# Kernel optimization log

Measured on AMD Instinct MI355X. Metric: run time of the kernel, lower is better.

Reference implementation:

```python
import jax, jax.numpy as jnp
import numpy as np

# Module hyperparameters (from __init__ defaults / init_kwargs)
A_PLUS = 0.005
A_MINUS = 0.00525
TAU_PLUS = 20.0
TAU_MINUS = 20.0
DT = 1.0

B, T, N_PRE, N_POST = 512, 100, 256, 256
SPIKE_RATE = 0.1


def setup_inputs() -> dict:
    key = jax.random.key(0)
    k1, k2, k3 = jax.random.split(key, 3)
    pre_spikes = (jax.random.uniform(k1, (B, T, N_PRE)) < SPIKE_RATE).astype(jnp.float32)
    post_spikes = (jax.random.uniform(k2, (B, T, N_POST)) < SPIKE_RATE).astype(jnp.float32)
    weights = jax.random.uniform(k3, (N_PRE, N_POST), dtype=jnp.float32)
    return {"pre_spikes": pre_spikes, "post_spikes": post_spikes, "weights": weights}


def _pre_trace(pre_tbn, decay):
    """trace[t] = sum_{tau=1..t} decay^tau * pre[t-tau]  (exact recurrence).

    pre_tbn: [T, B, N]. Returns [T, B, N] with trace[0] = 0.
    """
    def step(carry, x_t):
        # emit trace[t] = carry, then carry' = decay * (carry + pre[t])
        return decay * (carry + x_t), carry
    _, trace = jax.lax.scan(step, jnp.zeros_like(pre_tbn[0]), pre_tbn)
    return trace


def reference(pre_spikes, post_spikes, weights):
    """Classical STDP weight update.

    With T <= int(tau_plus*5) the original nested t/tau loops equal:
      dW[p,q] = (1/(B*T)) * sum_{t,b} (A+ * trace+[t,b,p] - A- * trace-[t,b,p]) * post[b,t,q]
    where trace+/- are exponential pre-synaptic eligibility traces.
    """
    batch, time_steps, _ = pre_spikes.shape
    pre_t = jnp.transpose(pre_spikes, (1, 0, 2))    # [T, B, n_pre]
    post_t = jnp.transpose(post_spikes, (1, 0, 2))  # [T, B, n_post]

    decay_plus = jnp.exp(jnp.float32(-DT / TAU_PLUS))
    decay_minus = jnp.exp(jnp.float32(-DT / TAU_MINUS))

    trace_plus = _pre_trace(pre_t, decay_plus)    # LTP: pre fires before post
    trace_minus = _pre_trace(pre_t, decay_minus)  # LTD: pre fires before post (depression of reversed pairing)

    eff = A_PLUS * trace_plus - A_MINUS * trace_minus  # [T, B, n_pre]
    weight_update = jnp.einsum('tbp,tbq->pq', eff, post_t) / (batch * time_steps)
    # original initializes update as zeros_like(weights); output shape matches weights
    return weight_update + jnp.zeros_like(weights)
```

## Files before the change

kernel.cpp:

```cpp
#include <hip/hip_runtime.h>
#include <stdint.h>

#define B_SZ   512
#define T_SZ   100
#define NPRE   256
#define NPOST  256
#define KTOT   (B_SZ * T_SZ)

typedef __bf16 bf16x8 __attribute__((ext_vector_type(8)));
typedef float  floatx4 __attribute__((ext_vector_type(4)));

__device__ __forceinline__ uint32_t bf16_rne(float v) {
    uint32_t bits = __float_as_uint(v);
    return (bits + 0x7FFFu + ((bits >> 16) & 1u)) >> 16;
}
__device__ __forceinline__ uint32_t pack_trunc2(float a, float b) {
    return (__float_as_uint(a) >> 16) | (__float_as_uint(b) & 0xFFFF0000u);
}

__global__ __launch_bounds__(512, 4) void stdp_fused_gemm(
    const float* __restrict__ pre, const float* __restrict__ post,
    float* __restrict__ partial)
{
    __shared__ __align__(16) unsigned short A_lds[32][512];
    __shared__ __align__(16) unsigned short B_lds[32][512];

    const int bx   = blockIdx.x;
    const int s    = bx & 127;
    const int tile = bx >> 7;
    const int pt   = tile & 1;
    const int qt   = tile >> 1;
    const int tid  = threadIdx.x;
    const int lane = tid & 63, wave = tid >> 6;
    const int l15 = lane & 15, l4 = lane >> 4;

    const int grp   = tid >> 7;
    const int p_loc = tid & 127;
    const int qloc  = tid & 127;
    const int qg = qloc >> 4, q15 = qloc & 15;
    const int pg = p_loc >> 4, lp = p_loc & 15;

    const float decay = 0.95122942450071400910f;

    uint32_t pk[50];
    {
        const int b = s * 4 + grp;
        const float* src = pre + (size_t)b * (T_SZ * NPRE) + pt * 128 + p_loc;
        float carry = 0.0f;
#pragma unroll
        for (int kc = 0; kc < 3; ++kc) {
            float x[32];
#pragma unroll
            for (int j = 0; j < 32; ++j)
                x[j] = src[(size_t)(kc * 32 + j) * NPRE];
#pragma unroll
            for (int j = 0; j < 16; ++j) {
                uint32_t lo = bf16_rne(carry);
                carry = decay * (carry + x[2 * j]);
                uint32_t hi = bf16_rne(carry);
                carry = decay * (carry + x[2 * j + 1]);
                pk[kc * 16 + j] = lo | (hi << 16);
            }
        }
        float x[4];
#pragma unroll
        for (int j = 0; j < 4; ++j)
            x[j] = src[(size_t)(96 + j) * NPRE];
#pragma unroll
        for (int j = 0; j < 2; ++j) {
            uint32_t lo = bf16_rne(carry);
            carry = decay * (carry + x[2 * j]);
            uint32_t hi = bf16_rne(carry);
            carry = decay * (carry + x[2 * j + 1]);
            pk[48 + j] = lo | (hi << 16);
        }
    }

    floatx4 acc[8] = {};

#pragma unroll
    for (int g = 0; g < 4; ++g) {
        const int b = s * 4 + g;
        if (g) __syncthreads();

        if (grp == g) {
#pragma unroll
            for (int kc = 0; kc < 3; ++kc)
#pragma unroll
                for (int w = 0; w < 4; ++w)
                    *(uint4*)&A_lds[kc * 8 + pg][(w * 16 + lp) * 8] =
                        make_uint4(pk[kc * 16 + w * 4],     pk[kc * 16 + w * 4 + 1],
                                   pk[kc * 16 + w * 4 + 2], pk[kc * 16 + w * 4 + 3]);
            *(uint4*)&A_lds[24 + pg][lp * 8] = make_uint4(pk[48], pk[49], 0u, 0u);
#pragma unroll
            for (int w = 1; w < 4; ++w)
                *(uint4*)&A_lds[24 + pg][(w * 16 + lp) * 8] =
                    make_uint4(0u, 0u, 0u, 0u);
        }

        const float* pb = post + (size_t)b * (T_SZ * NPOST) + qt * 128 + qloc;
        if (grp < 3) {
#pragma unroll
            for (int h = 0; h < 2; ++h) {
                float x[16];
#pragma unroll
                for (int j = 0; j < 16; ++j)
                    x[j] = pb[(size_t)(grp * 32 + h * 16 + j) * NPOST];
#pragma unroll
                for (int w2 = 0; w2 < 2; ++w2) {
                    const int w = h * 2 + w2;
                    *(uint4*)&B_lds[grp * 8 + qg][(w * 16 + q15) * 8] =
                        make_uint4(pack_trunc2(x[w2 * 8 + 0], x[w2 * 8 + 1]),
                                   pack_trunc2(x[w2 * 8 + 2], x[w2 * 8 + 3]),
                                   pack_trunc2(x[w2 * 8 + 4], x[w2 * 8 + 5]),
                                   pack_trunc2(x[w2 * 8 + 6], x[w2 * 8 + 7]));
                }
            }
        } else {
            float x[4];
#pragma unroll
            for (int j = 0; j < 4; ++j)
                x[j] = pb[(size_t)(96 + j) * NPOST];
            *(uint4*)&B_lds[24 + qg][q15 * 8] =
                make_uint4(pack_trunc2(x[0], x[1]), pack_trunc2(x[2], x[3]), 0u, 0u);
#pragma unroll
            for (int w = 1; w < 4; ++w)
                *(uint4*)&B_lds[24 + qg][(w * 16 + q15) * 8] =
                    make_uint4(0u, 0u, 0u, 0u);
        }
        __syncthreads();

#pragma unroll
        for (int kc = 0; kc < 4; ++kc) {
            bf16x8 a = *(const bf16x8*)&A_lds[kc * 8 + wave][lane * 8];
            bf16x8 bb[8];
#pragma unroll
            for (int gg = 0; gg < 8; ++gg)
                bb[gg] = *(const bf16x8*)&B_lds[kc * 8 + gg][lane * 8];
#pragma unroll
            for (int gg = 0; gg < 8; ++gg)
                acc[gg] = __builtin_amdgcn_mfma_f32_16x16x32_bf16(
                    a, bb[gg], acc[gg], 0, 0, 0);
        }
    }

    float* pout = partial + (size_t)bx * (128 * 128);
    const int r0 = wave * 16 + l4 * 4;
#pragma unroll
    for (int gg = 0; gg < 8; ++gg) {
        const int c = gg * 16 + l15;
#pragma unroll
        for (int v = 0; v < 4; ++v)
            pout[(size_t)(r0 + v) * 128 + c] = acc[gg][v];
    }
}

__global__ __launch_bounds__(256) void stdp_reduce1(
    const float* __restrict__ partial, float* __restrict__ tmp)
{
    const int t = blockIdx.x * 256 + threadIdx.x;
    const int g = t >> 16;
    const int e = t & 65535;
    const int tile = e >> 14;
    const float* src = partial + ((size_t)(tile * 128 + g * 16) << 14) + (e & 16383);
    float a4[4] = {};
#pragma unroll
    for (int i = 0; i < 4; ++i)
#pragma unroll
        for (int u = 0; u < 4; ++u)
            a4[u] += src[(size_t)(u * 4 + i) << 14];
    tmp[t] = (a4[0] + a4[1]) + (a4[2] + a4[3]);
}

__global__ __launch_bounds__(256) void stdp_reduce2(
    const float* __restrict__ tmp, float* __restrict__ out)
{
    const int idx = blockIdx.x * 256 + threadIdx.x;
    const int P = idx >> 8, Q = idx & 255;
    const int tile = (Q >> 7) * 2 + (P >> 7);
    const int e = (tile << 14) | ((P & 127) << 7) | (Q & 127);
    float a[4];
#pragma unroll
    for (int u = 0; u < 4; ++u)
        a[u] = tmp[(size_t)(2 * u) * 65536 + e] +
               tmp[(size_t)(2 * u + 1) * 65536 + e];
    const float scale = (0.005f - 0.00525f) * (1.0f / (float)KTOT);
    out[idx] = ((a[0] + a[1]) + (a[2] + a[3])) * scale;
}

extern "C" void kernel_launch(void* const* d_in, const int* in_sizes, int n_in,
                              void* d_out, int out_size, void* d_ws, size_t ws_size,
                              hipStream_t stream)
{
    const float* pre  = (const float*)d_in[0];
    const float* post = (const float*)d_in[1];
    float* out = (float*)d_out;

    float* partial = (float*)d_ws;
    float* tmp     = (float*)((char*)d_ws + (size_t)33554432);

    stdp_fused_gemm<<<512, 512, 0, stream>>>(pre, post, partial);
    stdp_reduce1<<<2048, 256, 0, stream>>>(partial, tmp);
    stdp_reduce2<<<256, 256, 0, stream>>>(tmp, out);
}
```

Measured before the change: 145.8 us.

## Double-buffer LDS tiles and use 1024-thread blocks covering eight batches each

The GEMM kernel now launches 256 blocks of 1024 threads. Each block handles eight batch items instead of four, and each wave computes a 16x64 output slice instead of 16x128. LDS tiles are double-buffered, so the next batch's post-spike loads are issued before the current MFMA work, which removes one barrier per step. With half as many blocks, the partial-sum buffer is halved and the first reduction reads fewer slices. The risks are lower occupancy from 1024-thread blocks and twice the LDS per block.

```diff
diff --git a/kernel.cpp b/kernel.cpp
--- a/kernel.cpp
+++ b/kernel.cpp
@@ -18,16 +18,69 @@
     return (__float_as_uint(a) >> 16) | (__float_as_uint(b) & 0xFFFF0000u);
 }
 
-__global__ __launch_bounds__(512, 4) void stdp_fused_gemm(
+__device__ __forceinline__ void deposit_A(unsigned short (*A)[512],
+                                          const uint32_t* pk, int pg, int lp)
+{
+#pragma unroll
+    for (int kc = 0; kc < 3; ++kc)
+#pragma unroll
+        for (int w = 0; w < 4; ++w)
+            *(uint4*)&A[kc * 8 + pg][(w * 16 + lp) * 8] =
+                make_uint4(pk[kc * 16 + w * 4],     pk[kc * 16 + w * 4 + 1],
+                           pk[kc * 16 + w * 4 + 2], pk[kc * 16 + w * 4 + 3]);
+    *(uint4*)&A[24 + pg][lp * 8] = make_uint4(pk[48], pk[49], 0u, 0u);
+#pragma unroll
+    for (int w = 1; w < 4; ++w)
+        *(uint4*)&A[24 + pg][(w * 16 + lp) * 8] = make_uint4(0u, 0u, 0u, 0u);
+}
+
+__device__ __forceinline__ void load_B(const float* pb, int grp, float* x)
+{
+    if (grp < 6) {
+#pragma unroll
+        for (int j = 0; j < 16; ++j)
+            x[j] = pb[(size_t)(16 * grp + j) * NPOST];
+    } else if (grp == 6) {
+#pragma unroll
+        for (int j = 0; j < 4; ++j)
+            x[j] = pb[(size_t)(96 + j) * NPOST];
+    }
+}
+__device__ __forceinline__ void store_B(unsigned short (*Bl)[512], int grp,
+                                        int qg, int q15, const float* x)
+{
+    if (grp < 6) {
+#pragma unroll
+        for (int h = 0; h < 2; ++h) {
+            const int o = 2 * grp + h;
+            *(uint4*)&Bl[(o >> 2) * 8 + qg][((o & 3) * 16 + q15) * 8] =
+                make_uint4(pack_trunc2(x[8 * h + 0], x[8 * h + 1]),
+                           pack_trunc2(x[8 * h + 2], x[8 * h + 3]),
+                           pack_trunc2(x[8 * h + 4], x[8 * h + 5]),
+                           pack_trunc2(x[8 * h + 6], x[8 * h + 7]));
+        }
+    } else if (grp == 6) {
+        *(uint4*)&Bl[24 + qg][q15 * 8] =
+            make_uint4(pack_trunc2(x[0], x[1]), pack_trunc2(x[2], x[3]), 0u, 0u);
+    } else {
+#pragma unroll
+        for (int o = 13; o < 16; ++o)
+            *(uint4*)&Bl[24 + qg][((o & 3) * 16 + q15) * 8] =
+                make_uint4(0u, 0u, 0u, 0u);
+    }
+}
+
+__global__ __launch_bounds__(1024) __attribute__((amdgpu_waves_per_eu(4, 4)))
+void stdp_fused_gemm(
     const float* __restrict__ pre, const float* __restrict__ post,
     float* __restrict__ partial)
 {
-    __shared__ __align__(16) unsigned short A_lds[32][512];
-    __shared__ __align__(16) unsigned short B_lds[32][512];
+    __shared__ __align__(16) unsigned short A_lds[2][32][512];
+    __shared__ __align__(16) unsigned short B_lds[2][32][512];
 
     const int bx   = blockIdx.x;
-    const int s    = bx & 127;
-    const int tile = bx >> 7;
+    const int s    = bx & 63;
+    const int tile = bx >> 6;
     const int pt   = tile & 1;
     const int qt   = tile >> 1;
     const int tid  = threadIdx.x;
@@ -39,12 +92,15 @@
     const int qloc  = tid & 127;
     const int qg = qloc >> 4, q15 = qloc & 15;
     const int pg = p_loc >> 4, lp = p_loc & 15;
+    const int wpg = wave >> 1;
+    const int wqh = wave & 1;
 
     const float decay = 0.95122942450071400910f;
+    const int b0 = s * 8;
 
     uint32_t pk[50];
     {
-        const int b = s * 4 + grp;
+        const int b = b0 + grp;
         const float* src = pre + (size_t)b * (T_SZ * NPRE) + pt * 128 + p_loc;
         float carry = 0.0f;
 #pragma unroll
@@ -76,79 +132,51 @@
         }
     }
 
-    floatx4 acc[8] = {};
-
-#pragma unroll
-    for (int g = 0; g < 4; ++g) {
-        const int b = s * 4 + g;
-        if (g) __syncthreads();
-
-        if (grp == g) {
-#pragma unroll
-            for (int kc = 0; kc < 3; ++kc)
-#pragma unroll
-                for (int w = 0; w < 4; ++w)
-                    *(uint4*)&A_lds[kc * 8 + pg][(w * 16 + lp) * 8] =
-                        make_uint4(pk[kc * 16 + w * 4],     pk[kc * 16 + w * 4 + 1],
-                                   pk[kc * 16 + w * 4 + 2], pk[kc * 16 + w * 4 + 3]);
-            *(uint4*)&A_lds[24 + pg][lp * 8] = make_uint4(pk[48], pk[49], 0u, 0u);
-#pragma unroll
-            for (int w = 1; w < 4; ++w)
-                *(uint4*)&A_lds[24 + pg][(w * 16 + lp) * 8] =
-                    make_uint4(0u, 0u, 0u, 0u);
-        }
-
-        const float* pb = post + (size_t)b * (T_SZ * NPOST) + qt * 128 + qloc;
-        if (grp < 3) {
-#pragma unroll
-            for (int h = 0; h < 2; ++h) {
-                float x[16];
-#pragma unroll
-                for (int j = 0; j < 16; ++j)
-                    x[j] = pb[(size_t)(grp * 32 + h * 16 + j) * NPOST];
-#pragma unroll
-                for (int w2 = 0; w2 < 2; ++w2) {
-                    const int w = h * 2 + w2;
-                    *(uint4*)&B_lds[grp * 8 + qg][(w * 16 + q15) * 8] =
-                        make_uint4(pack_trunc2(x[w2 * 8 + 0], x[w2 * 8 + 1]),
-                                   pack_trunc2(x[w2 * 8 + 2], x[w2 * 8 + 3]),
-                                   pack_trunc2(x[w2 * 8 + 4], x[w2 * 8 + 5]),
-                                   pack_trunc2(x[w2 * 8 + 6], x[w2 * 8 + 7]));
-                }
-            }
-        } else {
-            float x[4];
-#pragma unroll
-            for (int j = 0; j < 4; ++j)
-                x[j] = pb[(size_t)(96 + j) * NPOST];
-            *(uint4*)&B_lds[24 + qg][q15 * 8] =
-                make_uint4(pack_trunc2(x[0], x[1]), pack_trunc2(x[2], x[3]), 0u, 0u);
-#pragma unroll
-            for (int w = 1; w < 4; ++w)
-                *(uint4*)&B_lds[24 + qg][(w * 16 + q15) * 8] =
-                    make_uint4(0u, 0u, 0u, 0u);
-        }
-        __syncthreads();
+    floatx4 acc[4] = {};
+
+    if (grp == 0) deposit_A(A_lds[0], pk, pg, lp);
+    {
+        float xb[16];
+        load_B(post + (size_t)b0 * (T_SZ * NPOST) + qt * 128 + qloc, grp, xb);
+        store_B(B_lds[0], grp, qg, q15, xb);
+    }
+    __syncthreads();
+
+#pragma unroll
+    for (int g = 0; g < 8; ++g) {
+        const int nb = g + 1;
+        const int cb = g & 1;
+
+        float xn[16];
+        if (nb < 8)
+            load_B(post + (size_t)(b0 + nb) * (T_SZ * NPOST) + qt * 128 + qloc,
+                   grp, xn);
 
 #pragma unroll
         for (int kc = 0; kc < 4; ++kc) {
-            bf16x8 a = *(const bf16x8*)&A_lds[kc * 8 + wave][lane * 8];
-            bf16x8 bb[8];
-#pragma unroll
-            for (int gg = 0; gg < 8; ++gg)
-                bb[gg] = *(const bf16x8*)&B_lds[kc * 8 + gg][lane * 8];
-#pragma unroll
-            for (int gg = 0; gg < 8; ++gg)
+            bf16x8 a = *(const bf16x8*)&A_lds[cb][kc * 8 + wpg][lane * 8];
+            bf16x8 bb[4];
+#pragma unroll
+            for (int gg = 0; gg < 4; ++gg)
+                bb[gg] = *(const bf16x8*)&B_lds[cb][kc * 8 + wqh * 4 + gg][lane * 8];
+#pragma unroll
+            for (int gg = 0; gg < 4; ++gg)
                 acc[gg] = __builtin_amdgcn_mfma_f32_16x16x32_bf16(
                     a, bb[gg], acc[gg], 0, 0, 0);
         }
+
+        if (nb < 8) {
+            if (grp == nb) deposit_A(A_lds[nb & 1], pk, pg, lp);
+            store_B(B_lds[nb & 1], grp, qg, q15, xn);
+            __syncthreads();
+        }
     }
 
     float* pout = partial + (size_t)bx * (128 * 128);
-    const int r0 = wave * 16 + l4 * 4;
-#pragma unroll
-    for (int gg = 0; gg < 8; ++gg) {
-        const int c = gg * 16 + l15;
+    const int r0 = wpg * 16 + l4 * 4;
+#pragma unroll
+    for (int gg = 0; gg < 4; ++gg) {
+        const int c = (wqh * 4 + gg) * 16 + l15;
 #pragma unroll
         for (int v = 0; v < 4; ++v)
             pout[(size_t)(r0 + v) * 128 + c] = acc[gg][v];
@@ -162,13 +190,13 @@
     const int g = t >> 16;
     const int e = t & 65535;
     const int tile = e >> 14;
-    const float* src = partial + ((size_t)(tile * 128 + g * 16) << 14) + (e & 16383);
+    const float* src = partial + ((size_t)(tile * 64 + g * 8) << 14) + (e & 16383);
     float a4[4] = {};
 #pragma unroll
-    for (int i = 0; i < 4; ++i)
+    for (int i = 0; i < 2; ++i)
 #pragma unroll
         for (int u = 0; u < 4; ++u)
-            a4[u] += src[(size_t)(u * 4 + i) << 14];
+            a4[u] += src[(size_t)(u * 2 + i) << 14];
     tmp[t] = (a4[0] + a4[1]) + (a4[2] + a4[3]);
 }
 
@@ -197,9 +225,9 @@
     float* out = (float*)d_out;
 
     float* partial = (float*)d_ws;
-    float* tmp     = (float*)((char*)d_ws + (size_t)33554432);
-
-    stdp_fused_gemm<<<512, 512, 0, stream>>>(pre, post, partial);
+    float* tmp     = (float*)((char*)d_ws + (size_t)16777216);
+
+    stdp_fused_gemm<<<256, 1024, 0, stream>>>(pre, post, partial);
     stdp_reduce1<<<2048, 256, 0, stream>>>(partial, tmp);
     stdp_reduce2<<<256, 256, 0, stream>>>(tmp, out);
 }
```

Result: no change. 144.2 us (-1.1%).

## Compute full 256x256 tile per block with double-buffered LDS staging

Applied to the files above, without the earlier changes.

The GEMM kernel now uses 1024-thread blocks. Each block covers the full 256x256 output for two batches instead of one 128x128 quadrant for four batches. Each input row is therefore read and trace-processed once rather than twice, using float2/float4 vectorized loads. A two-buffer LDS pipeline overlaps staging of the next 32-step chunk with the MFMA work on the current one. The cost is a per-block partial output twice as large, which doubles the traffic of the reduction kernels. Only 6 of the 16 waves do the serial trace and conversion staging, which could leave the pipeline latency-bound.

```diff
diff --git a/kernel.cpp b/kernel.cpp
--- a/kernel.cpp
+++ b/kernel.cpp
@@ -18,141 +18,144 @@
     return (__float_as_uint(a) >> 16) | (__float_as_uint(b) & 0xFFFF0000u);
 }
 
-__global__ __launch_bounds__(512, 4) void stdp_fused_gemm(
+__global__ __launch_bounds__(1024, 4) void stdp_fused_gemm(
     const float* __restrict__ pre, const float* __restrict__ post,
     float* __restrict__ partial)
 {
-    __shared__ __align__(16) unsigned short A_lds[32][512];
-    __shared__ __align__(16) unsigned short B_lds[32][512];
+    __shared__ __align__(16) unsigned short A_lds[2][16][512];
+    __shared__ __align__(16) unsigned short B_lds[2][16][512];
 
     const int bx   = blockIdx.x;
-    const int s    = bx & 127;
-    const int tile = bx >> 7;
-    const int pt   = tile & 1;
-    const int qt   = tile >> 1;
     const int tid  = threadIdx.x;
     const int lane = tid & 63, wave = tid >> 6;
     const int l15 = lane & 15, l4 = lane >> 4;
 
-    const int grp   = tid >> 7;
-    const int p_loc = tid & 127;
-    const int qloc  = tid & 127;
-    const int qg = qloc >> 4, q15 = qloc & 15;
-    const int pg = p_loc >> 4, lp = p_loc & 15;
-
     const float decay = 0.95122942450071400910f;
-
-    uint32_t pk[50];
-    {
-        const int b = s * 4 + grp;
-        const float* src = pre + (size_t)b * (T_SZ * NPRE) + pt * 128 + p_loc;
-        float carry = 0.0f;
-#pragma unroll
-        for (int kc = 0; kc < 3; ++kc) {
-            float x[32];
-#pragma unroll
-            for (int j = 0; j < 32; ++j)
-                x[j] = src[(size_t)(kc * 32 + j) * NPRE];
-#pragma unroll
-            for (int j = 0; j < 16; ++j) {
-                uint32_t lo = bf16_rne(carry);
-                carry = decay * (carry + x[2 * j]);
-                uint32_t hi = bf16_rne(carry);
-                carry = decay * (carry + x[2 * j + 1]);
-                pk[kc * 16 + j] = lo | (hi << 16);
-            }
+    const int b0 = 2 * bx;
+
+    float c0 = 0.0f, c1 = 0.0f;
+
+    const int p0  = (wave & 1) * 128 + 2 * lane;
+    const int apg = p0 >> 4, ap15 = p0 & 15;
+    const int bg  = wave - 2;
+    const int qg  = lane >> 2, q15 = (4 * lane) & 15;
+
+    floatx4 acc[4][4] = {};
+
+#define STAGE_A(BUF, BT, CK)                                                   \
+    {                                                                          \
+        const int b_ = b0 + (BT);                                              \
+        if ((CK) == 0) { c0 = 0.0f; c1 = 0.0f; }                               \
+        const float* rb_ = pre + (size_t)b_ * (T_SZ * NPRE) +                  \
+                           (wave & 1) * 128 + 2 * lane;                        \
+        _Pragma("unroll")                                                      \
+        for (int og_ = 0; og_ < 4; ++og_) {                                    \
+            float xx_[16];                                                     \
+            _Pragma("unroll")                                                  \
+            for (int j_ = 0; j_ < 8; ++j_) {                                   \
+                const int t_ = (CK) * 32 + og_ * 8 + j_;                       \
+                if (t_ < T_SZ) {                                               \
+                    float2 v_ = *(const float2*)(rb_ + (size_t)t_ * NPRE);     \
+                    xx_[2 * j_] = v_.x; xx_[2 * j_ + 1] = v_.y;                \
+                } else { xx_[2 * j_] = 0.0f; xx_[2 * j_ + 1] = 0.0f; }         \
+            }                                                                  \
+            uint32_t u0_[4], u1_[4];                                           \
+            _Pragma("unroll")                                                  \
+            for (int m_ = 0; m_ < 4; ++m_) {                                   \
+                uint32_t lo0_ = bf16_rne(c0);                                  \
+                c0 = decay * (c0 + xx_[4 * m_ + 0]);                           \
+                uint32_t lo1_ = bf16_rne(c1);                                  \
+                c1 = decay * (c1 + xx_[4 * m_ + 1]);                           \
+                uint32_t hi0_ = bf16_rne(c0);                                  \
+                c0 = decay * (c0 + xx_[4 * m_ + 2]);                           \
+                uint32_t hi1_ = bf16_rne(c1);                                  \
+                c1 = decay * (c1 + xx_[4 * m_ + 3]);                           \
+                u0_[m_] = lo0_ | (hi0_ << 16);                                 \
+                u1_[m_] = lo1_ | (hi1_ << 16);                                 \
+            }                                                                  \
+            *(uint4*)&A_lds[BUF][apg][(og_ * 16 + ap15) * 8] =                 \
+                make_uint4(u0_[0], u0_[1], u0_[2], u0_[3]);                    \
+            *(uint4*)&A_lds[BUF][apg][(og_ * 16 + ap15 + 1) * 8] =             \
+                make_uint4(u1_[0], u1_[1], u1_[2], u1_[3]);                    \
+        }                                                                      \
+    }
+
+#define STAGE_B(BUF, BT, CK)                                                   \
+    {                                                                          \
+        const int b_ = b0 + (BT);                                              \
+        const float* rb_ = post + (size_t)b_ * (T_SZ * NPOST) + 4 * lane;      \
+        float xx_[8][4];                                                       \
+        _Pragma("unroll")                                                      \
+        for (int j_ = 0; j_ < 8; ++j_) {                                       \
+            const int t_ = (CK) * 32 + bg * 8 + j_;                            \
+            if (t_ < T_SZ) {                                                   \
+                float4 v_ = *(const float4*)(rb_ + (size_t)t_ * NPOST);        \
+                xx_[j_][0] = v_.x; xx_[j_][1] = v_.y;                          \
+                xx_[j_][2] = v_.z; xx_[j_][3] = v_.w;                          \
+            } else {                                                           \
+                xx_[j_][0] = 0.0f; xx_[j_][1] = 0.0f;                          \
+                xx_[j_][2] = 0.0f; xx_[j_][3] = 0.0f;                          \
+            }                                                                  \
+        }                                                                      \
+        _Pragma("unroll")                                                      \
+        for (int c_ = 0; c_ < 4; ++c_) {                                       \
+            uint32_t u_[4];                                                    \
+            _Pragma("unroll")                                                  \
+            for (int m_ = 0; m_ < 4; ++m_)                                     \
+                u_[m_] = pack_trunc2(xx_[2 * m_][c_], xx_[2 * m_ + 1][c_]);    \
+            *(uint4*)&B_lds[BUF][qg][(bg * 16 + q15 + c_) * 8] =               \
+                make_uint4(u_[0], u_[1], u_[2], u_[3]);                        \
+        }                                                                      \
+    }
+
+#define MFMA_STEP(BUF)                                                         \
+    {                                                                          \
+        bf16x8 af_[4], bf_[4];                                                 \
+        _Pragma("unroll")                                                      \
+        for (int f_ = 0; f_ < 4; ++f_) {                                       \
+            af_[f_] = *(const bf16x8*)&A_lds[BUF][(wave >> 2) * 4 + f_]        \
+                                           [lane * 8];                         \
+            bf_[f_] = *(const bf16x8*)&B_lds[BUF][(wave & 3) * 4 + f_]         \
+                                           [lane * 8];                         \
+        }                                                                      \
+        _Pragma("unroll")                                                      \
+        for (int fa_ = 0; fa_ < 4; ++fa_)                                      \
+            _Pragma("unroll")                                                  \
+            for (int fb_ = 0; fb_ < 4; ++fb_)                                  \
+                acc[fa_][fb_] = __builtin_amdgcn_mfma_f32_16x16x32_bf16(       \
+                    af_[fa_], bf_[fb_], acc[fa_][fb_], 0, 0, 0);               \
+    }
+
+    if (wave < 2)      STAGE_A(0, 0, 0)
+    else if (wave < 6) STAGE_B(0, 0, 0)
+    __syncthreads();
+
+#pragma unroll
+    for (int k = 0; k < 8; ++k) {
+        const int cur = k & 1, nxt = cur ^ 1;
+        if (k < 7) {
+            if (wave < 2)      STAGE_A(nxt, (k + 1) >> 2, (k + 1) & 3)
+            else if (wave < 6) STAGE_B(nxt, (k + 1) >> 2, (k + 1) & 3)
         }
-        float x[4];
-#pragma unroll
-        for (int j = 0; j < 4; ++j)
-            x[j] = src[(size_t)(96 + j) * NPRE];
-#pragma unroll
-        for (int j = 0; j < 2; ++j) {
-            uint32_t lo = bf16_rne(carry);
-            carry = decay * (carry + x[2 * j]);
-            uint32_t hi = bf16_rne(carry);
-            carry = decay * (carry + x[2 * j + 1]);
-            pk[48 + j] = lo | (hi << 16);
+        MFMA_STEP(cur)
+        __syncthreads();
+    }
+
+    float* pout = partial + (size_t)bx * (256 * 256);
+#pragma unroll
+    for (int fa = 0; fa < 4; ++fa) {
+        const int r0 = (wave >> 2) * 64 + fa * 16 + l4 * 4;
+#pragma unroll
+        for (int fb = 0; fb < 4; ++fb) {
+            const int c = (wave & 3) * 64 + fb * 16 + l15;
+#pragma unroll
+            for (int v = 0; v < 4; ++v)
+                pout[(size_t)(r0 + v) * 256 + c] = acc[fa][fb][v];
         }
     }
-
-    floatx4 acc[8] = {};
-
-#pragma unroll
-    for (int g = 0; g < 4; ++g) {
-        const int b = s * 4 + g;
-        if (g) __syncthreads();
-
-        if (grp == g) {
-#pragma unroll
-            for (int kc = 0; kc < 3; ++kc)
-#pragma unroll
-                for (int w = 0; w < 4; ++w)
-                    *(uint4*)&A_lds[kc * 8 + pg][(w * 16 + lp) * 8] =
-                        make_uint4(pk[kc * 16 + w * 4],     pk[kc * 16 + w * 4 + 1],
-                                   pk[kc * 16 + w * 4 + 2], pk[kc * 16 + w * 4 + 3]);
-            *(uint4*)&A_lds[24 + pg][lp * 8] = make_uint4(pk[48], pk[49], 0u, 0u);
-#pragma unroll
-            for (int w = 1; w < 4; ++w)
-                *(uint4*)&A_lds[24 + pg][(w * 16 + lp) * 8] =
-                    make_uint4(0u, 0u, 0u, 0u);
-        }
-
-        const float* pb = post + (size_t)b * (T_SZ * NPOST) + qt * 128 + qloc;
-        if (grp < 3) {
-#pragma unroll
-            for (int h = 0; h < 2; ++h) {
-                float x[16];
-#pragma unroll
-                for (int j = 0; j < 16; ++j)
-                    x[j] = pb[(size_t)(grp * 32 + h * 16 + j) * NPOST];
-#pragma unroll
-                for (int w2 = 0; w2 < 2; ++w2) {
-                    const int w = h * 2 + w2;
-                    *(uint4*)&B_lds[grp * 8 + qg][(w * 16 + q15) * 8] =
-                        make_uint4(pack_trunc2(x[w2 * 8 + 0], x[w2 * 8 + 1]),
-                                   pack_trunc2(x[w2 * 8 + 2], x[w2 * 8 + 3]),
-                                   pack_trunc2(x[w2 * 8 + 4], x[w2 * 8 + 5]),
-                                   pack_trunc2(x[w2 * 8 + 6], x[w2 * 8 + 7]));
-                }
-            }
-        } else {
-            float x[4];
-#pragma unroll
-            for (int j = 0; j < 4; ++j)
-                x[j] = pb[(size_t)(96 + j) * NPOST];
-            *(uint4*)&B_lds[24 + qg][q15 * 8] =
-                make_uint4(pack_trunc2(x[0], x[1]), pack_trunc2(x[2], x[3]), 0u, 0u);
-#pragma unroll
-            for (int w = 1; w < 4; ++w)
-                *(uint4*)&B_lds[24 + qg][(w * 16 + q15) * 8] =
-                    make_uint4(0u, 0u, 0u, 0u);
-        }
-        __syncthreads();
-
-#pragma unroll
-        for (int kc = 0; kc < 4; ++kc) {
-            bf16x8 a = *(const bf16x8*)&A_lds[kc * 8 + wave][lane * 8];
-            bf16x8 bb[8];
-#pragma unroll
-            for (int gg = 0; gg < 8; ++gg)
-                bb[gg] = *(const bf16x8*)&B_lds[kc * 8 + gg][lane * 8];
-#pragma unroll
-            for (int gg = 0; gg < 8; ++gg)
-                acc[gg] = __builtin_amdgcn_mfma_f32_16x16x32_bf16(
-                    a, bb[gg], acc[gg], 0, 0, 0);
-        }
-    }
-
-    float* pout = partial + (size_t)bx * (128 * 128);
-    const int r0 = wave * 16 + l4 * 4;
-#pragma unroll
-    for (int gg = 0; gg < 8; ++gg) {
-        const int c = gg * 16 + l15;
-#pragma unroll
-        for (int v = 0; v < 4; ++v)
-            pout[(size_t)(r0 + v) * 128 + c] = acc[gg][v];
-    }
+#undef STAGE_A
+#undef STAGE_B
+#undef MFMA_STEP
 }
 
 __global__ __launch_bounds__(256) void stdp_reduce1(
@@ -161,14 +164,13 @@
     const int t = blockIdx.x * 256 + threadIdx.x;
     const int g = t >> 16;
     const int e = t & 65535;
-    const int tile = e >> 14;
-    const float* src = partial + ((size_t)(tile * 128 + g * 16) << 14) + (e & 16383);
+    const float* src = partial + ((size_t)g * 32) * 65536 + e;
     float a4[4] = {};
 #pragma unroll
-    for (int i = 0; i < 4; ++i)
+    for (int i = 0; i < 8; ++i)
 #pragma unroll
         for (int u = 0; u < 4; ++u)
-            a4[u] += src[(size_t)(u * 4 + i) << 14];
+            a4[u] += src[(size_t)(i * 4 + u) * 65536];
     tmp[t] = (a4[0] + a4[1]) + (a4[2] + a4[3]);
 }
 
@@ -176,14 +178,11 @@
     const float* __restrict__ tmp, float* __restrict__ out)
 {
     const int idx = blockIdx.x * 256 + threadIdx.x;
-    const int P = idx >> 8, Q = idx & 255;
-    const int tile = (Q >> 7) * 2 + (P >> 7);
-    const int e = (tile << 14) | ((P & 127) << 7) | (Q & 127);
     float a[4];
 #pragma unroll
     for (int u = 0; u < 4; ++u)
-        a[u] = tmp[(size_t)(2 * u) * 65536 + e] +
-               tmp[(size_t)(2 * u + 1) * 65536 + e];
+        a[u] = tmp[(size_t)(2 * u) * 65536 + idx] +
+               tmp[(size_t)(2 * u + 1) * 65536 + idx];
     const float scale = (0.005f - 0.00525f) * (1.0f / (float)KTOT);
     out[idx] = ((a[0] + a[1]) + (a[2] + a[3])) * scale;
 }
@@ -197,9 +196,9 @@
     float* out = (float*)d_out;
 
     float* partial = (float*)d_ws;
-    float* tmp     = (float*)((char*)d_ws + (size_t)33554432);
-
-    stdp_fused_gemm<<<512, 512, 0, stream>>>(pre, post, partial);
+    float* tmp     = (float*)((char*)d_ws + (size_t)67108864);
+
+    stdp_fused_gemm<<<256, 1024, 0, stream>>>(pre, post, partial);
     stdp_reduce1<<<2048, 256, 0, stream>>>(partial, tmp);
     stdp_reduce2<<<256, 256, 0, stream>>>(tmp, out);
 }
```

Result: slower. 154.8 us (+6.2%).

## Pipeline spike loads via async global-to-LDS double buffering with wider output tiles

Applied to the files above, without the earlier changes.

Restructures the fused trace+GEMM kernel to use 1024-thread blocks that each cover a 128x256 output tile. Raw fp32 spikes are streamed into LDS with async global_load_lds in a two-chunk double buffer, and some threads then convert them into bf16 MFMA fragments while the next chunk is in flight. This targets exposed global-load latency and cuts the redundant reloading of pre spikes across q tiles, since the block count is halved. It adds more barriers per chunk, and each block's trace computation is serialized onto 128 threads.

```diff
diff --git a/kernel.cpp b/kernel.cpp
--- a/kernel.cpp
+++ b/kernel.cpp
@@ -18,140 +18,163 @@
     return (__float_as_uint(a) >> 16) | (__float_as_uint(b) & 0xFFFF0000u);
 }
 
-__global__ __launch_bounds__(512, 4) void stdp_fused_gemm(
+__device__ __forceinline__ void async_ld16(float* lds, const float* g) {
+    __builtin_amdgcn_global_load_lds(
+        (const __attribute__((address_space(1))) unsigned int*)g,
+        (__attribute__((address_space(3))) unsigned int*)lds,
+        16, 0, 0);
+}
+
+__device__ __forceinline__ void issue_chunk(
+    const float* __restrict__ pre, const float* __restrict__ post,
+    int b0, int pt, int wave, int lane,
+    float* rawA_buf , float* rawB_buf , int ck)
+{
+    const int bi = ck >> 2, cc = ck & 3;
+    const float* pa = pre  + (size_t)(b0 + bi) * (T_SZ * NPRE)
+                           + (size_t)(cc * 32) * NPRE + pt * 128;
+    const float* pb = post + (size_t)(b0 + bi) * (T_SZ * NPOST)
+                           + (size_t)(cc * 32) * NPOST;
+    {
+        const int rp = (cc < 3) ? wave : (wave < 1 ? wave : 1);
+        const float* g = pa + (size_t)(2 * rp + (lane >> 5)) * NPRE + (lane & 31) * 4;
+        async_ld16(rawA_buf + 2 * rp * 128, g);
+    }
+#pragma unroll
+    for (int h = 0; h < 2; ++h) {
+        const int r  = wave + 16 * h;
+        const int rr = (cc < 3) ? r : (r < 3 ? r : 3);
+        const float* g = pb + (size_t)rr * NPOST + lane * 4;
+        async_ld16(rawB_buf + rr * 256, g);
+    }
+}
+
+__global__ __launch_bounds__(1024) __attribute__((amdgpu_waves_per_eu(4, 4)))
+void stdp_fused_gemm(
     const float* __restrict__ pre, const float* __restrict__ post,
     float* __restrict__ partial)
 {
-    __shared__ __align__(16) unsigned short A_lds[32][512];
-    __shared__ __align__(16) unsigned short B_lds[32][512];
+    __shared__ __align__(16) float rawA[2][32][128];
+    __shared__ __align__(16) float rawB[2][32][256];
+    __shared__ __align__(16) unsigned short Afrag[8][512];
+    __shared__ __align__(16) unsigned short Bfrag[16][512];
 
     const int bx   = blockIdx.x;
     const int s    = bx & 127;
-    const int tile = bx >> 7;
-    const int pt   = tile & 1;
-    const int qt   = tile >> 1;
+    const int pt   = bx >> 7;
     const int tid  = threadIdx.x;
     const int lane = tid & 63, wave = tid >> 6;
     const int l15 = lane & 15, l4 = lane >> 4;
-
-    const int grp   = tid >> 7;
-    const int p_loc = tid & 127;
-    const int qloc  = tid & 127;
-    const int qg = qloc >> 4, q15 = qloc & 15;
-    const int pg = p_loc >> 4, lp = p_loc & 15;
+    const int b0 = s * 4;
 
     const float decay = 0.95122942450071400910f;
 
-    uint32_t pk[50];
-    {
-        const int b = s * 4 + grp;
-        const float* src = pre + (size_t)b * (T_SZ * NPRE) + pt * 128 + p_loc;
-        float carry = 0.0f;
-#pragma unroll
-        for (int kc = 0; kc < 3; ++kc) {
-            float x[32];
-#pragma unroll
-            for (int j = 0; j < 32; ++j)
-                x[j] = src[(size_t)(kc * 32 + j) * NPRE];
-#pragma unroll
-            for (int j = 0; j < 16; ++j) {
-                uint32_t lo = bf16_rne(carry);
-                carry = decay * (carry + x[2 * j]);
-                uint32_t hi = bf16_rne(carry);
-                carry = decay * (carry + x[2 * j + 1]);
-                pk[kc * 16 + j] = lo | (hi << 16);
+    floatx4 acc[2][4] = {};
+    float carry = 0.0f;
+
+    issue_chunk(pre, post, b0, pt, wave, lane,
+                &rawA[0][0][0], &rawB[0][0][0], 0);
+    issue_chunk(pre, post, b0, pt, wave, lane,
+                &rawA[1][0][0], &rawB[1][0][0], 1);
+    __builtin_amdgcn_sched_barrier(0);
+
+#pragma unroll
+    for (int k = 0; k < 16; ++k) {
+        const int cb = k & 1;
+        const int cc = k & 3;
+
+        if (k < 15) asm volatile("s_waitcnt vmcnt(3)" ::: "memory");
+        else        asm volatile("s_waitcnt vmcnt(0)" ::: "memory");
+        __builtin_amdgcn_sched_barrier(0);
+        __builtin_amdgcn_s_barrier();
+
+        if (tid < 128) {
+            if (cc == 0) carry = 0.0f;
+            const int p15 = tid & 15, pgq = tid >> 4;
+#pragma unroll
+            for (int w = 0; w < 4; ++w) {
+                float xv[8];
+#pragma unroll
+                for (int j = 0; j < 8; ++j) {
+                    const int tt = cc * 32 + w * 8 + j;
+                    xv[j] = (tt < T_SZ) ? rawA[cb][w * 8 + j][tid] : 0.0f;
+                }
+                uint32_t u[4];
+#pragma unroll
+                for (int m = 0; m < 4; ++m) {
+                    uint32_t lo = bf16_rne(carry);
+                    carry = decay * (carry + xv[2 * m]);
+                    uint32_t hi = bf16_rne(carry);
+                    carry = decay * (carry + xv[2 * m + 1]);
+                    u[m] = lo | (hi << 16);
+                }
+                *(uint4*)&Afrag[pgq][(w * 16 + p15) * 8] =
+                    make_uint4(u[0], u[1], u[2], u[3]);
             }
-        }
-        float x[4];
-#pragma unroll
-        for (int j = 0; j < 4; ++j)
-            x[j] = src[(size_t)(96 + j) * NPRE];
-#pragma unroll
-        for (int j = 0; j < 2; ++j) {
-            uint32_t lo = bf16_rne(carry);
-            carry = decay * (carry + x[2 * j]);
-            uint32_t hi = bf16_rne(carry);
-            carry = decay * (carry + x[2 * j + 1]);
-            pk[48 + j] = lo | (hi << 16);
-        }
-    }
-
-    floatx4 acc[8] = {};
-
-#pragma unroll
-    for (int g = 0; g < 4; ++g) {
-        const int b = s * 4 + g;
-        if (g) __syncthreads();
-
-        if (grp == g) {
-#pragma unroll
-            for (int kc = 0; kc < 3; ++kc)
-#pragma unroll
-                for (int w = 0; w < 4; ++w)
-                    *(uint4*)&A_lds[kc * 8 + pg][(w * 16 + lp) * 8] =
-                        make_uint4(pk[kc * 16 + w * 4],     pk[kc * 16 + w * 4 + 1],
-                                   pk[kc * 16 + w * 4 + 2], pk[kc * 16 + w * 4 + 3]);
-            *(uint4*)&A_lds[24 + pg][lp * 8] = make_uint4(pk[48], pk[49], 0u, 0u);
-#pragma unroll
-            for (int w = 1; w < 4; ++w)
-                *(uint4*)&A_lds[24 + pg][(w * 16 + lp) * 8] =
-                    make_uint4(0u, 0u, 0u, 0u);
-        }
-
-        const float* pb = post + (size_t)b * (T_SZ * NPOST) + qt * 128 + qloc;
-        if (grp < 3) {
-#pragma unroll
-            for (int h = 0; h < 2; ++h) {
-                float x[16];
-#pragma unroll
-                for (int j = 0; j < 16; ++j)
-                    x[j] = pb[(size_t)(grp * 32 + h * 16 + j) * NPOST];
-#pragma unroll
-                for (int w2 = 0; w2 < 2; ++w2) {
-                    const int w = h * 2 + w2;
-                    *(uint4*)&B_lds[grp * 8 + qg][(w * 16 + q15) * 8] =
-                        make_uint4(pack_trunc2(x[w2 * 8 + 0], x[w2 * 8 + 1]),
-                                   pack_trunc2(x[w2 * 8 + 2], x[w2 * 8 + 3]),
-                                   pack_trunc2(x[w2 * 8 + 4], x[w2 * 8 + 5]),
-                                   pack_trunc2(x[w2 * 8 + 6], x[w2 * 8 + 7]));
+        } else if (tid < 640) {
+            const int idx = tid - 128, q = idx & 255, th = idx >> 8;
+            const int q15 = q & 15, qgq = q >> 4;
+#pragma unroll
+            for (int w2 = 0; w2 < 2; ++w2) {
+                const int w = th * 2 + w2;
+                float yv[8];
+#pragma unroll
+                for (int j = 0; j < 8; ++j) {
+                    const int tt = cc * 32 + w * 8 + j;
+                    yv[j] = (tt < T_SZ) ? rawB[cb][w * 8 + j][q] : 0.0f;
                 }
+                uint32_t u[4];
+#pragma unroll
+                for (int m = 0; m < 4; ++m)
+                    u[m] = pack_trunc2(yv[2 * m], yv[2 * m + 1]);
+                *(uint4*)&Bfrag[qgq][(w * 16 + q15) * 8] =
+                    make_uint4(u[0], u[1], u[2], u[3]);
             }
-        } else {
-            float x[4];
-#pragma unroll
-            for (int j = 0; j < 4; ++j)
-                x[j] = pb[(size_t)(96 + j) * NPOST];
-            *(uint4*)&B_lds[24 + qg][q15 * 8] =
-                make_uint4(pack_trunc2(x[0], x[1]), pack_trunc2(x[2], x[3]), 0u, 0u);
-#pragma unroll
-            for (int w = 1; w < 4; ++w)
-                *(uint4*)&B_lds[24 + qg][(w * 16 + q15) * 8] =
-                    make_uint4(0u, 0u, 0u, 0u);
-        }
-        __syncthreads();
-
-#pragma unroll
-        for (int kc = 0; kc < 4; ++kc) {
-            bf16x8 a = *(const bf16x8*)&A_lds[kc * 8 + wave][lane * 8];
-            bf16x8 bb[8];
-#pragma unroll
-            for (int gg = 0; gg < 8; ++gg)
-                bb[gg] = *(const bf16x8*)&B_lds[kc * 8 + gg][lane * 8];
-#pragma unroll
-            for (int gg = 0; gg < 8; ++gg)
-                acc[gg] = __builtin_amdgcn_mfma_f32_16x16x32_bf16(
-                    a, bb[gg], acc[gg], 0, 0, 0);
-        }
-    }
-
-    float* pout = partial + (size_t)bx * (128 * 128);
-    const int r0 = wave * 16 + l4 * 4;
-#pragma unroll
-    for (int gg = 0; gg < 8; ++gg) {
-        const int c = gg * 16 + l15;
-#pragma unroll
-        for (int v = 0; v < 4; ++v)
-            pout[(size_t)(r0 + v) * 128 + c] = acc[gg][v];
+        }
+
+        asm volatile("s_waitcnt lgkmcnt(0)" ::: "memory");
+        __builtin_amdgcn_sched_barrier(0);
+        __builtin_amdgcn_s_barrier();
+
+        if (k < 14) {
+            issue_chunk(pre, post, b0, pt, wave, lane,
+                        &rawA[cb][0][0], &rawB[cb][0][0], k + 2);
+            __builtin_amdgcn_sched_barrier(0);
+        }
+
+        {
+            bf16x8 af[2], bf[4];
+#pragma unroll
+            for (int f = 0; f < 2; ++f)
+                af[f] = *(const bf16x8*)&Afrag[(wave >> 2) * 2 + f][lane * 8];
+#pragma unroll
+            for (int g = 0; g < 4; ++g)
+                bf[g] = *(const bf16x8*)&Bfrag[(wave & 3) * 4 + g][lane * 8];
+#pragma unroll
+            for (int f = 0; f < 2; ++f)
+#pragma unroll
+                for (int g = 0; g < 4; ++g)
+                    acc[f][g] = __builtin_amdgcn_mfma_f32_16x16x32_bf16(
+                        af[f], bf[g], acc[f][g], 0, 0, 0);
+        }
+
+        if (k < 15) {
+            __builtin_amdgcn_sched_barrier(0);
+            __builtin_amdgcn_s_barrier();
+        }
+    }
+
+    float* pout = partial + (size_t)bx * (128 * 256);
+#pragma unroll
+    for (int f = 0; f < 2; ++f) {
+        const int r0 = (wave >> 2) * 32 + f * 16 + l4 * 4;
+#pragma unroll
+        for (int g = 0; g < 4; ++g) {
+            const int c = (wave & 3) * 64 + g * 16 + l15;
+#pragma unroll
+            for (int v = 0; v < 4; ++v)
+                pout[(size_t)(r0 + v) * 256 + c] = acc[f][g][v];
+        }
     }
 }
 
@@ -161,14 +184,14 @@
     const int t = blockIdx.x * 256 + threadIdx.x;
     const int g = t >> 16;
     const int e = t & 65535;
-    const int tile = e >> 14;
-    const float* src = partial + ((size_t)(tile * 128 + g * 16) << 14) + (e & 16383);
+    const float* src = partial + (size_t)(e >> 15) * 4194304 + (e & 32767)
+                               + (size_t)(g * 16) * 32768;
     float a4[4] = {};
 #pragma unroll
     for (int i = 0; i < 4; ++i)
 #pragma unroll
         for (int u = 0; u < 4; ++u)
-            a4[u] += src[(size_t)(u * 4 + i) << 14];
+            a4[u] += src[(size_t)(u * 4 + i) * 32768];
     tmp[t] = (a4[0] + a4[1]) + (a4[2] + a4[3]);
 }
 
@@ -176,14 +199,11 @@
     const float* __restrict__ tmp, float* __restrict__ out)
 {
     const int idx = blockIdx.x * 256 + threadIdx.x;
-    const int P = idx >> 8, Q = idx & 255;
-    const int tile = (Q >> 7) * 2 + (P >> 7);
-    const int e = (tile << 14) | ((P & 127) << 7) | (Q & 127);
     float a[4];
 #pragma unroll
     for (int u = 0; u < 4; ++u)
-        a[u] = tmp[(size_t)(2 * u) * 65536 + e] +
-               tmp[(size_t)(2 * u + 1) * 65536 + e];
+        a[u] = tmp[(size_t)(2 * u) * 65536 + idx] +
+               tmp[(size_t)(2 * u + 1) * 65536 + idx];
     const float scale = (0.005f - 0.00525f) * (1.0f / (float)KTOT);
     out[idx] = ((a[0] + a[1]) + (a[2] + a[3])) * scale;
 }
@@ -199,7 +219,7 @@
     float* partial = (float*)d_ws;
     float* tmp     = (float*)((char*)d_ws + (size_t)33554432);
 
-    stdp_fused_gemm<<<512, 512, 0, stream>>>(pre, post, partial);
+    stdp_fused_gemm<<<256, 1024, 0, stream>>>(pre, post, partial);
     stdp_reduce1<<<2048, 256, 0, stream>>>(partial, tmp);
     stdp_reduce2<<<256, 256, 0, stream>>>(tmp, out);
 }
```

Result: no change. 145.3 us (-0.3%).
